# Optimization experiments

Measured on AMD Instinct MI355X. Metric: run time of the kernel, lower is better.

Reference implementation:

```python
import jax, jax.numpy as jnp
import numpy as np


def conv2d(x, w, b, pad):
    out = jax.lax.conv_general_dilated(x, w, (1, 1), ((pad, pad), (pad, pad)),
                                       dimension_numbers=('NCHW', 'OIHW', 'NCHW'))
    return out + b[None, :, None, None]


def silu(x):
    return x * jax.nn.sigmoid(x)


def group_norm(x, g, b, groups, eps=1e-5):
    B, C, H, W = x.shape
    xg = x.reshape(B, groups, C // groups, H, W)
    m = xg.mean(axis=(2, 3, 4), keepdims=True)
    v = xg.var(axis=(2, 3, 4), keepdims=True)
    xg = (xg - m) * jax.lax.rsqrt(v + eps)
    return xg.reshape(B, C, H, W) * g[None, :, None, None] + b[None, :, None, None]


def snake_cumsum(off):
    # off: [B,K,H,W]. Center kernel point has zero offset; points accumulate
    # outward from center (the 'snake' bend), as in DSCNet.
    K = off.shape[1]
    c = K // 2
    upper = jnp.cumsum(off[:, c + 1:], axis=1)
    lower = jnp.flip(jnp.cumsum(jnp.flip(off[:, :c], axis=1), axis=1), axis=1)
    return jnp.concatenate([lower, jnp.zeros_like(off[:, :1]), upper], axis=1)


def bilinear_gather(img, ys, xs):
    # img [B,C,H,W]; ys,xs [B,K,H,W] float coords -> sampled [B,C,K,H,W]
    B, C, H, W = img.shape
    K = ys.shape[1]
    ys = jnp.clip(ys, 0.0, H - 1.0)
    xs = jnp.clip(xs, 0.0, W - 1.0)
    y0f = jnp.floor(ys)
    x0f = jnp.floor(xs)
    wy = (ys - y0f)[:, None]  # [B,1,K,H,W]
    wx = (xs - x0f)[:, None]
    y0 = y0f.astype(jnp.int32)
    x0 = x0f.astype(jnp.int32)
    y1 = jnp.minimum(y0 + 1, H - 1)
    x1 = jnp.minimum(x0 + 1, W - 1)
    flat = img.reshape(B, C, H * W)

    def gat(yi, xi):
        idx = (yi * W + xi).reshape(B, -1)  # [B, K*H*W]
        g = jnp.take_along_axis(flat, idx[:, None, :], axis=2)
        return g.reshape(B, C, K, H, W)

    return (gat(y0, x0) * (1 - wy) * (1 - wx) + gat(y0, x1) * (1 - wy) * wx
            + gat(y1, x0) * wy * (1 - wx) + gat(y1, x1) * wy * wx)


def dsconv(x, off_w, off_b, dsc_w, dsc_b, gn_g, gn_b, morph, extend_scope=1.0):
    # Dynamic snake conv for one morphology.
    # morph 0: kernel spreads along x, bends in y; morph 1: opposite.
    B, C, H, W = x.shape
    K = dsc_w.shape[-1]
    c = K // 2
    off = jnp.tanh(conv2d(x, off_w, off_b, pad=1))  # [B,2K,H,W]; BN folded into conv bias
    bend = snake_cumsum(off[:, :K] if morph == 0 else off[:, K:])  # [B,K,H,W]
    spread = (jnp.arange(K) - c).astype(x.dtype)[None, :, None, None]
    hh = jnp.arange(H, dtype=x.dtype)[None, None, :, None]
    ww = jnp.arange(W, dtype=x.dtype)[None, None, None, :]
    if morph == 0:
        ys = hh + extend_scope * bend
        xs = jnp.broadcast_to(ww + spread, ys.shape)
    else:
        xs = ww + extend_scope * bend
        ys = jnp.broadcast_to(hh + spread, xs.shape)
    sampled = bilinear_gather(x, ys, xs)  # [B,C,K,H,W]
    # k-point conv over the stacked snake axis == (K,1)/(1,K) conv with stride K
    out = jnp.einsum('bckhw,ock->bohw', sampled, dsc_w) + dsc_b[None, :, None, None]
    O = dsc_w.shape[0]
    return jax.nn.relu(group_norm(out, gn_g, gn_b, groups=O // 4))


def dysnake_conv(x, p):
    # DySnakeConv: standard conv + snake-x + snake-y, concat, 1x1 fuse
    kpad = p['conv0_w'].shape[-1] // 2
    a = silu(conv2d(x, p['conv0_w'], p['conv0_b'], pad=kpad))
    bx = dsconv(x, p['offx_w'], p['offx_b'], p['dscx_w'], p['dscx_b'], p['gnx_g'], p['gnx_b'], morph=0)
    by = dsconv(x, p['offy_w'], p['offy_b'], p['dscy_w'], p['dscy_b'], p['gny_g'], p['gny_b'], morph=1)
    cat = jnp.concatenate([a, bx, by], axis=1)  # [B,3*ouc,H,W]
    return silu(jnp.einsum('bchw,oc->bohw', cat, p['fuse_w']) + p['fuse_b'][None, :, None, None])


_PNAMES = ['conv0_w', 'conv0_b', 'offx_w', 'offx_b', 'dscx_w', 'dscx_b', 'gnx_g', 'gnx_b',
           'offy_w', 'offy_b', 'dscy_w', 'dscy_b', 'gny_g', 'gny_b', 'fuse_w', 'fuse_b']


def setup_inputs() -> dict:
    key = jax.random.key(0)
    ks = iter(jax.random.split(key, 64))

    def rn(shape, s=0.05):
        return jax.random.normal(next(ks), shape, dtype=jnp.float32) * s

    B, H, W = 8, 80, 80
    c1, c2, c_ = 256, 256, 128
    kk = 3

    def block(inc, ouc, pre):
        return {
            pre + 'conv0_w': rn((ouc, inc, kk, kk)), pre + 'conv0_b': rn((ouc,)),
            pre + 'offx_w': rn((2 * kk, inc, 3, 3)), pre + 'offx_b': rn((2 * kk,)),
            pre + 'dscx_w': rn((ouc, inc, kk)), pre + 'dscx_b': rn((ouc,)),
            pre + 'gnx_g': jnp.ones((ouc,), jnp.float32), pre + 'gnx_b': jnp.zeros((ouc,), jnp.float32),
            pre + 'offy_w': rn((2 * kk, inc, 3, 3)), pre + 'offy_b': rn((2 * kk,)),
            pre + 'dscy_w': rn((ouc, inc, kk)), pre + 'dscy_b': rn((ouc,)),
            pre + 'gny_g': jnp.ones((ouc,), jnp.float32), pre + 'gny_b': jnp.zeros((ouc,), jnp.float32),
            pre + 'fuse_w': rn((ouc, 3 * ouc)), pre + 'fuse_b': rn((ouc,)),
        }

    inp = {'x': jax.random.normal(next(ks), (B, c1, H, W), dtype=jnp.float32)}
    inp.update(block(c1, c_, 'cv1_'))
    inp.update(block(c_, c2, 'cv2_'))
    return inp


def reference(x, cv1_conv0_w, cv1_conv0_b, cv1_offx_w, cv1_offx_b, cv1_dscx_w, cv1_dscx_b,
              cv1_gnx_g, cv1_gnx_b, cv1_offy_w, cv1_offy_b, cv1_dscy_w, cv1_dscy_b,
              cv1_gny_g, cv1_gny_b, cv1_fuse_w, cv1_fuse_b,
              cv2_conv0_w, cv2_conv0_b, cv2_offx_w, cv2_offx_b, cv2_dscx_w, cv2_dscx_b,
              cv2_gnx_g, cv2_gnx_b, cv2_offy_w, cv2_offy_b, cv2_dscy_w, cv2_dscy_b,
              cv2_gny_g, cv2_gny_b, cv2_fuse_w, cv2_fuse_b):
    p1 = dict(zip(_PNAMES, (cv1_conv0_w, cv1_conv0_b, cv1_offx_w, cv1_offx_b, cv1_dscx_w, cv1_dscx_b,
                            cv1_gnx_g, cv1_gnx_b, cv1_offy_w, cv1_offy_b, cv1_dscy_w, cv1_dscy_b,
                            cv1_gny_g, cv1_gny_b, cv1_fuse_w, cv1_fuse_b)))
    p2 = dict(zip(_PNAMES, (cv2_conv0_w, cv2_conv0_b, cv2_offx_w, cv2_offx_b, cv2_dscx_w, cv2_dscx_b,
                            cv2_gnx_g, cv2_gnx_b, cv2_offy_w, cv2_offy_b, cv2_dscy_w, cv2_dscy_b,
                            cv2_gny_g, cv2_gny_b, cv2_fuse_w, cv2_fuse_b)))
    h = dysnake_conv(x, p1)
    h = dysnake_conv(h, p2)
    return x + h  # shortcut and c1 == c2
```

## Files before the change

kernel.cpp:

```cpp
#include <hip/hip_runtime.h>
#include <cstddef>

#define B_   8
#define H_   80
#define W_   80
#define HW   6400
#define W2   82
#define HW2  6724

typedef __attribute__((ext_vector_type(8)))  short short8;
typedef __attribute__((ext_vector_type(16))) float f32x16;

__device__ __forceinline__ float bf2f(ushort u) {
    return __uint_as_float(((unsigned)u) << 16);
}
__device__ __forceinline__ ushort f2bf(float f) {
    unsigned u = __float_as_uint(f);
    u += 0x7FFF + ((u >> 16) & 1);
    return (ushort)(u >> 16);
}
__device__ __forceinline__ f32x16 mfma16(short8 a, short8 b, f32x16 c) {
    return __builtin_amdgcn_mfma_f32_32x32x16_bf16(a, b, c, 0, 0, 0);
}
__device__ __forceinline__ void async16(const void* g, void* l) {
    __builtin_amdgcn_global_load_lds(
        (const __attribute__((address_space(1))) unsigned int*)g,
        (__attribute__((address_space(3))) unsigned int*)l, 16, 0, 0);
}
__device__ __forceinline__ const ushort* frag_ptr(const ushort* sbuf, int row, int c8l) {
    return sbuf + row * 64 + ((c8l ^ (row & 7)) << 3);
}

__global__ __launch_bounds__(256) void transpose_x_kernel(
    const float* __restrict__ x, ushort* __restrict__ xp, int C) {
    __shared__ float s[64][65];
    int hw0 = blockIdx.x * 64, c0 = blockIdx.y * 64, b = blockIdx.z;
    int t = threadIdx.x;
    int hl = t & 63, cq = t >> 6;
    #pragma unroll
    for (int i = 0; i < 16; i++) {
        int cl = cq * 16 + i;
        s[cl][hl] = x[((size_t)(b * C + c0 + cl)) * HW + hw0 + hl];
    }
    __syncthreads();
    int cl = t & 63, hq = t >> 6;
    #pragma unroll
    for (int i = 0; i < 16; i++) {
        int hl2 = hq * 16 + i;
        int hw = hw0 + hl2;
        int h = hw / W_, w = hw - h * W_;
        xp[((size_t)(b * HW2 + (h + 1) * W2 + w + 1)) * C + c0 + cl] = f2bf(s[cl][hl2]);
    }
}

__global__ __launch_bounds__(256) void final_add_kernel(
    const float* __restrict__ x, const ushort* __restrict__ h2,
    float* __restrict__ out, int C) {
    __shared__ float s[64][65];
    int hw0 = blockIdx.x * 64, c0 = blockIdx.y * 64, b = blockIdx.z;
    int t = threadIdx.x;
    int cl = t & 63, hq = t >> 6;
    #pragma unroll
    for (int i = 0; i < 16; i++) {
        int hl = hq * 16 + i;
        s[cl][hl] = bf2f(h2[((size_t)(b * HW + hw0 + hl)) * C + c0 + cl]);
    }
    __syncthreads();
    int hl = t & 63, cq = t >> 6;
    #pragma unroll
    for (int i = 0; i < 16; i++) {
        int cl2 = cq * 16 + i;
        size_t o = ((size_t)(b * C + c0 + cl2)) * HW + hw0 + hl;
        out[o] = x[o] + s[cl2][hl];
    }
}

__global__ void wprep_kernel(const float* __restrict__ src,
                             ushort* __restrict__ dst, int OC, int CIN, int T) {
    int idx = blockIdx.x * 256 + threadIdx.x;
    if (idx >= OC * CIN * T) return;
    int oc = idx / (CIN * T);
    int r = idx - oc * CIN * T;
    int ci = r / T, t_ = r - ci * T;
    dst[((size_t)oc * T + t_) * CIN + ci] = f2bf(src[idx]);
}

__global__ void wprep_off_kernel(const float* __restrict__ wx_,
                                 const float* __restrict__ bx_,
                                 const float* __restrict__ wy_,
                                 const float* __restrict__ by_,
                                 ushort* __restrict__ dst,
                                 float* __restrict__ bdst, int CIN) {
    int idx = blockIdx.x * 256 + threadIdx.x;
    if (idx < 4) {
        const int chs[4] = {0, 2, 3, 5};
        bdst[idx] = (idx < 2) ? bx_[chs[idx]] : by_[chs[idx]];
    }
    if (idx >= 32 * 9 * CIN) return;
    int oc = idx / (9 * CIN);
    int r = idx - oc * 9 * CIN;
    int tap = r / CIN, ci = r - tap * CIN;
    float v = 0.f;
    if (oc < 4) {
        const int chs[4] = {0, 2, 3, 5};
        const float* src = (oc < 2) ? wx_ : wy_;
        v = src[((size_t)chs[oc] * CIN + ci) * 9 + tap];
    }
    dst[idx] = f2bf(v);
}

__global__ __launch_bounds__(256, 2) void off_conv_mfma_kernel(
    const ushort* __restrict__ xp, const ushort* __restrict__ wB,
    const float* __restrict__ bias, float* __restrict__ off4, int CIN) {
    __shared__ ushort s_x[162 * 64];
    __shared__ ushort s_w[144 * 64];
    int tid = threadIdx.x;
    int ty0 = (blockIdx.x / 5) * 16, tx0 = (blockIdx.x % 5) * 16;
    int b = blockIdx.y;
    int lane = tid & 63, wid = tid >> 6;
    int l31 = lane & 31, kg = lane >> 5;
    int pym[2], pxm[2];
    #pragma unroll
    for (int mf = 0; mf < 2; mf++) {
        int p = wid * 64 + mf * 32 + l31;
        pym[mf] = p >> 4; pxm[mf] = p & 15;
    }
    f32x16 acc[2] = {};
    for (int c0 = 0; c0 < CIN; c0 += 32) {
        __syncthreads();
        for (int u = tid; u < 1296; u += 256) {
            int pid = u >> 2, ci8 = u & 3;
            int r = pid / 18, c = pid - r * 18;
            int py = ty0 + r, px = tx0 + c;
            uint4 v = *(const uint4*)(xp + ((size_t)(b * HW2 + py * W2 + px)) * CIN
                                      + c0 + ci8 * 8);
            int row = pid >> 1;
            int phys = (((pid & 1) << 2) + ci8) ^ (row & 7);
            *(uint4*)(s_x + row * 64 + phys * 8) = v;
        }
        for (int cc = wid; cc < 18; cc += 4) {
            int L = cc * 64 + lane;
            int row = L >> 3, phys = L & 7;
            int logical = phys ^ (row & 7);
            int tap = row >> 4, ocp = row & 15;
            int oc = ocp * 2 + (logical >> 2), ci8 = logical & 3;
            async16(wB + ((size_t)oc * 9 + tap) * CIN + c0 + ci8 * 8,
                    s_w + (size_t)L * 8);
        }
        __syncthreads();
        #pragma unroll
        for (int tap = 0; tap < 9; tap++) {
            int dy = tap / 3, dx = tap - dy * 3;
            int wrow = tap * 16 + (l31 >> 1);
            #pragma unroll
            for (int ks = 0; ks < 2; ks++) {
                int blk = ks * 2 + kg;
                int wphys = (((l31 & 1) << 2) + blk) ^ (wrow & 7);
                short8 bfr = *(const short8*)(s_w + wrow * 64 + wphys * 8);
                #pragma unroll
                for (int mf = 0; mf < 2; mf++) {
                    int pix = (pym[mf] + dy) * 18 + (pxm[mf] + dx);
                    int xrow = pix >> 1;
                    int xphys = (((pix & 1) << 2) + blk) ^ (xrow & 7);
                    short8 afr = *(const short8*)(s_x + xrow * 64 + xphys * 8);
                    acc[mf] = mfma16(afr, bfr, acc[mf]);
                }
            }
        }
    }
    int oc = l31;
    if (oc < 4) {
        float bb = bias[oc];
        #pragma unroll
        for (int mf = 0; mf < 2; mf++) {
            #pragma unroll
            for (int reg = 0; reg < 16; reg++) {
                int row = (reg & 3) + 8 * (reg >> 2) + 4 * kg;
                int p = wid * 64 + mf * 32 + row;
                int y = ty0 + (p >> 4), x = tx0 + (p & 15);
                off4[((size_t)b * 4 + oc) * HW + y * W_ + x] = tanhf(acc[mf][reg] + bb);
            }
        }
    }
}

__global__ __launch_bounds__(256, 4) void conv3x3_gemm_kernel(
    const ushort* __restrict__ xp, const ushort* __restrict__ wB,
    const float* __restrict__ bias, ushort* __restrict__ out,
    int CIN, int OC) {
    __shared__ ushort s_a[128 * 64];
    __shared__ ushort s_b[128 * 64];
    int tid = threadIdx.x;
    int m0 = blockIdx.x * 128, n0 = blockIdx.y * 128;
    int b = m0 / HW, hw0 = m0 - b * HW;
    int lane = tid & 63, wid = tid >> 6;
    int l31 = lane & 31, kg = lane >> 5;
    int wm = wid >> 1, wn = wid & 1;
    const ushort* xpb = xp + (size_t)b * HW2 * CIN;
    const ushort* asrc[4];
    #pragma unroll
    for (int j = 0; j < 4; j++) {
        int s = (wid * 4 + j) * 64 + lane;
        int r = s >> 3, c8p = s & 7;
        int c8l = c8p ^ (r & 7);
        int hw = hw0 + r;
        int h = hw / W_, w = hw - h * W_;
        asrc[j] = xpb + ((size_t)((h + 1) * W2 + (w + 1))) * CIN + c8l * 8;
    }
    f32x16 acc[2][2] = {};
    int K = 9 * CIN, nk = K >> 6;
    int tap = 0, cioff = 0;
    for (int kc = 0; kc < nk; kc++) {
        int kg64 = kc << 6;
        int dy = tap / 3, dx = tap - dy * 3;
        int soff = ((dy - 1) * W2 + (dx - 1)) * CIN + cioff;
        __syncthreads();
        #pragma unroll
        for (int j = 0; j < 4; j++) {
            int s = (wid * 4 + j) * 64 + lane;
            int r = s >> 3, c8p = s & 7;
            int c8l = c8p ^ (r & 7);
            async16(wB + (size_t)(n0 + r) * K + kg64 + c8l * 8, s_b + s * 8);
            async16(asrc[j] + soff, s_a + s * 8);
        }
        __syncthreads();
        #pragma unroll
        for (int ks = 0; ks < 4; ks++) {
            int c8l = ks * 2 + kg;
            short8 af0 = *(const short8*)frag_ptr(s_a, wm * 64 + l31, c8l);
            short8 af1 = *(const short8*)frag_ptr(s_a, wm * 64 + 32 + l31, c8l);
            short8 bf0 = *(const short8*)frag_ptr(s_b, wn * 64 + l31, c8l);
            short8 bf1 = *(const short8*)frag_ptr(s_b, wn * 64 + 32 + l31, c8l);
            acc[0][0] = mfma16(af0, bf0, acc[0][0]);
            acc[0][1] = mfma16(af0, bf1, acc[0][1]);
            acc[1][0] = mfma16(af1, bf0, acc[1][0]);
            acc[1][1] = mfma16(af1, bf1, acc[1][1]);
        }
        cioff += 64;
        if (cioff == CIN) { cioff = 0; tap++; }
    }
    #pragma unroll
    for (int nf = 0; nf < 2; nf++) {
        int n = n0 + wn * 64 + nf * 32 + l31;
        float bb = bias[n];
        #pragma unroll
        for (int mf = 0; mf < 2; mf++) {
            #pragma unroll
            for (int reg = 0; reg < 16; reg++) {
                int row = (reg & 3) + 8 * (reg >> 2) + 4 * kg;
                int m = m0 + wm * 64 + mf * 32 + row;
                float v = acc[mf][nf][reg] + bb;
                v = v / (1.f + expf(-v));
                out[(size_t)m * OC + n] = f2bf(v);
            }
        }
    }
}

__global__ __launch_bounds__(256, 4) void dsc_gemm_kernel(
    const ushort* __restrict__ xp, const float* __restrict__ off4,
    const ushort* __restrict__ Bwx, const float* __restrict__ biasx,
    ushort* __restrict__ outx,
    const ushort* __restrict__ Bwy, const float* __restrict__ biasy,
    ushort* __restrict__ outy, float* __restrict__ stat, int CIN, int OC) {
    __shared__ ushort s_a[128 * 64];
    __shared__ ushort s_b[128 * 64];
    __shared__ int   s_i0[3][128];
    __shared__ int   s_i1[3][128];
    __shared__ float s_wl[3][128];
    int tid = threadIdx.x;
    int morph = blockIdx.z;
    const ushort* Bw = morph ? Bwy : Bwx;
    const float* bias = morph ? biasy : biasx;
    ushort* out = morph ? outy : outx;
    float* statm = stat + (size_t)morph * B_ * 256 * 2;
    int m0 = blockIdx.x * 128, n0 = blockIdx.y * 128;
    int b = m0 / HW, hw0 = m0 - b * HW;
    for (int u = tid; u < 384; u += 256) {
        int k3 = u >> 7, r = u & 127;
        int hw = hw0 + r;
        int h = hw / W_, w = hw - h * W_;
        float bend = 0.f;
        if (k3 != 1) {
            int mp = (morph ? 2 : 0) + (k3 >> 1);
            bend = off4[((size_t)b * 4 + mp) * HW + hw];
        }
        int i0, i1; float wl;
        if (morph == 0) {
            float ys = fminf(fmaxf((float)h + bend, 0.f), 79.f);
            float y0f = floorf(ys); wl = ys - y0f;
            int y0 = (int)y0f, y1 = min(y0 + 1, 79);
            int xk = min(max(w + k3 - 1, 0), 79);
            i0 = (y0 + 1) * W2 + xk + 1; i1 = (y1 + 1) * W2 + xk + 1;
        } else {
            float xs = fminf(fmaxf((float)w + bend, 0.f), 79.f);
            float x0f = floorf(xs); wl = xs - x0f;
            int x0 = (int)x0f, x1 = min(x0 + 1, 79);
            int yk = min(max(h + k3 - 1, 0), 79);
            i0 = (yk + 1) * W2 + x0 + 1; i1 = (yk + 1) * W2 + x1 + 1;
        }
        s_i0[k3][r] = i0; s_i1[k3][r] = i1; s_wl[k3][r] = wl;
    }
    int lane = tid & 63, wid = tid >> 6;
    int l31 = lane & 31, kg = lane >> 5;
    int wm = wid >> 1, wn = wid & 1;
    f32x16 acc[2][2] = {};
    int K = 3 * CIN, nk = K >> 6;
    const ushort* xb = xp + (size_t)b * HW2 * CIN;
    for (int kc = 0; kc < nk; kc++) {
        int kg64 = kc << 6;
        int k3 = kg64 / CIN;
        int cioff = kg64 - k3 * CIN;
        __syncthreads();
        #pragma unroll
        for (int j = 0; j < 4; j++) {
            int s = (wid * 4 + j) * 64 + lane;
            int r = s >> 3, c8p = s & 7;
            int c8l = c8p ^ (r & 7);
            async16(Bw + (size_t)(n0 + r) * K + kg64 + c8l * 8, s_b + s * 8);
        }
        #pragma unroll
        for (int i = 0; i < 4; i++) {
            int s = i * 256 + tid;
            int r = s >> 3, c8p = s & 7;
            int c8l = c8p ^ (r & 7);
            int ci = cioff + c8l * 8;
            float wl = s_wl[k3][r];
            uint4 u0 = *(const uint4*)(xb + (size_t)s_i0[k3][r] * CIN + ci);
            uint4 u1 = *(const uint4*)(xb + (size_t)s_i1[k3][r] * CIN + ci);
            const ushort* p0 = (const ushort*)&u0;
            const ushort* p1 = (const ushort*)&u1;
            ushort tv[8];
            #pragma unroll
            for (int j = 0; j < 8; j++) {
                float f0 = bf2f(p0[j]);
                tv[j] = f2bf(f0 + (bf2f(p1[j]) - f0) * wl);
            }
            *(uint4*)(s_a + s * 8) = *(uint4*)tv;
        }
        __syncthreads();
        #pragma unroll
        for (int ks = 0; ks < 4; ks++) {
            int c8l = ks * 2 + kg;
            short8 af0 = *(const short8*)frag_ptr(s_a, wm * 64 + l31, c8l);
            short8 af1 = *(const short8*)frag_ptr(s_a, wm * 64 + 32 + l31, c8l);
            short8 bf0 = *(const short8*)frag_ptr(s_b, wn * 64 + l31, c8l);
            short8 bf1 = *(const short8*)frag_ptr(s_b, wn * 64 + 32 + l31, c8l);
            acc[0][0] = mfma16(af0, bf0, acc[0][0]);
            acc[0][1] = mfma16(af0, bf1, acc[0][1]);
            acc[1][0] = mfma16(af1, bf0, acc[1][0]);
            acc[1][1] = mfma16(af1, bf1, acc[1][1]);
        }
    }
    #pragma unroll
    for (int nf = 0; nf < 2; nf++) {
        int n = n0 + wn * 64 + nf * 32 + l31;
        float bb = bias[n];
        float ssum = 0.f, ssq = 0.f;
        #pragma unroll
        for (int mf = 0; mf < 2; mf++) {
            #pragma unroll
            for (int reg = 0; reg < 16; reg++) {
                int row = (reg & 3) + 8 * (reg >> 2) + 4 * kg;
                int m = m0 + wm * 64 + mf * 32 + row;
                float v = acc[mf][nf][reg] + bb;
                ssum += v; ssq += v * v;
                out[(size_t)m * OC + n] = f2bf(v);
            }
        }
        ssum += __shfl_xor(ssum, 32);
        ssq  += __shfl_xor(ssq, 32);
        if (kg == 0) {
            float* st = statm + ((size_t)b * OC + n) * 2;
            atomicAdd(st, ssum);
            atomicAdd(st + 1, ssq);
        }
    }
}

__global__ __launch_bounds__(256, 4) void gemm128_kernel(
    const ushort* __restrict__ a0, const ushort* __restrict__ a1,
    const ushort* __restrict__ a2, int part_k,
    const ushort* __restrict__ Bw, int K, int N,
    const float* __restrict__ bias, ushort* __restrict__ out, int epi_silu,
    int out_pad) {
    __shared__ ushort s_a[128 * 64];
    __shared__ ushort s_b[128 * 64];
    int tid = threadIdx.x;
    int m0 = blockIdx.x * 128, n0 = blockIdx.y * 128;
    int lane = tid & 63, wid = tid >> 6;
    int l31 = lane & 31, kg = lane >> 5;
    int wm = wid >> 1, wn = wid & 1;
    f32x16 acc[2][2] = {};
    int nk = K >> 6;
    for (int kc = 0; kc < nk; kc++) {
        int kg64 = kc << 6;
        int part = kg64 / part_k;
        int koff = kg64 - part * part_k;
        const ushort* ap = (part == 0) ? a0 : (part == 1 ? a1 : a2);
        __syncthreads();
        #pragma unroll
        for (int j = 0; j < 4; j++) {
            int s = (wid * 4 + j) * 64 + lane;
            int r = s >> 3, c8p = s & 7;
            int c8l = c8p ^ (r & 7);
            async16(ap + (size_t)(m0 + r) * part_k + koff + c8l * 8, s_a + s * 8);
            async16(Bw + (size_t)(n0 + r) * K + kg64 + c8l * 8, s_b + s * 8);
        }
        __syncthreads();
        #pragma unroll
        for (int ks = 0; ks < 4; ks++) {
            int c8l = ks * 2 + kg;
            short8 af0 = *(const short8*)frag_ptr(s_a, wm * 64 + l31, c8l);
            short8 af1 = *(const short8*)frag_ptr(s_a, wm * 64 + 32 + l31, c8l);
            short8 bf0 = *(const short8*)frag_ptr(s_b, wn * 64 + l31, c8l);
            short8 bf1 = *(const short8*)frag_ptr(s_b, wn * 64 + 32 + l31, c8l);
            acc[0][0] = mfma16(af0, bf0, acc[0][0]);
            acc[0][1] = mfma16(af0, bf1, acc[0][1]);
            acc[1][0] = mfma16(af1, bf0, acc[1][0]);
            acc[1][1] = mfma16(af1, bf1, acc[1][1]);
        }
    }
    #pragma unroll
    for (int nf = 0; nf < 2; nf++) {
        int n = n0 + wn * 64 + nf * 32 + l31;
        float bb = bias[n];
        #pragma unroll
        for (int mf = 0; mf < 2; mf++) {
            #pragma unroll
            for (int reg = 0; reg < 16; reg++) {
                int row = (reg & 3) + 8 * (reg >> 2) + 4 * kg;
                int m = m0 + wm * 64 + mf * 32 + row;
                float v = acc[mf][nf][reg] + bb;
                if (epi_silu) v = v / (1.f + expf(-v));
                size_t mm = (size_t)m;
                if (out_pad) {
                    int bb_ = m / HW, hw = m - bb_ * HW;
                    int h = hw / W_, w = hw - h * W_;
                    mm = (size_t)bb_ * HW2 + (h + 1) * W2 + w + 1;
                }
                out[mm * N + n] = f2bf(v);
            }
        }
    }
}

__global__ void gn_finalize_kernel(const float* __restrict__ stat,
                                   const float* __restrict__ gx,
                                   const float* __restrict__ bx,
                                   const float* __restrict__ gy,
                                   const float* __restrict__ by,
                                   float* __restrict__ scx, float* __restrict__ shx,
                                   float* __restrict__ scy, float* __restrict__ shy,
                                   int C) {
    int idx = blockIdx.x * 256 + threadIdx.x;
    if (idx >= B_ * C) return;
    int which = blockIdx.y;
    const float* gamma = which ? gy : gx;
    const float* beta  = which ? by : bx;
    float* sc = which ? scy : scx;
    float* sh = which ? shy : shx;
    int b = idx / C, c = idx - b * C;
    const float* st = stat + (size_t)which * B_ * 256 * 2
                    + ((size_t)b * C + (c & ~3)) * 2;
    float s  = st[0] + st[2] + st[4] + st[6];
    float sq = st[1] + st[3] + st[5] + st[7];
    float mean = s / (4.f * HW);
    float var = sq / (4.f * HW) - mean * mean;
    float rs = rsqrtf(var + 1e-5f);
    float scale = rs * gamma[c];
    sc[idx] = scale;
    sh[idx] = beta[c] - mean * scale;
}

__global__ __launch_bounds__(256) void gn_apply_kernel(
    ushort* __restrict__ bqx, ushort* __restrict__ bqy,
    const float* __restrict__ scx, const float* __restrict__ shx,
    const float* __restrict__ scy, const float* __restrict__ shy, int C) {
    ushort* bq = blockIdx.y ? bqy : bqx;
    const float* sc = blockIdx.y ? scy : scx;
    const float* sh = blockIdx.y ? shy : shx;
    size_t e = ((size_t)blockIdx.x * 256 + threadIdx.x) * 8;
    int c = (int)(e % C);
    int b = (int)(e / ((size_t)HW * C));
    const float* scb = sc + (size_t)b * C + c;
    const float* shb = sh + (size_t)b * C + c;
    uint4 v = *(const uint4*)(bq + e);
    const ushort* sv = (const ushort*)&v;
    ushort tv[8];
    #pragma unroll
    for (int j = 0; j < 8; j++)
        tv[j] = f2bf(fmaxf(bf2f(sv[j]) * scb[j] + shb[j], 0.f));
    *(uint4*)(bq + e) = *(uint4*)tv;
}

struct BlkBuf {
    ushort *xp, *abuf, *bqx, *bqy, *hout;
    float *off4, *stat, *scx, *shx, *scy, *shy, *boff;
    ushort *wc, *wdx, *wdy, *wf, *woff;
};

static void run_block(const BlkBuf& B, int CIN, int OC,
                      const float* const* P, int out_pad, hipStream_t stream) {
    dim3 blk(256);
    hipMemsetAsync(B.stat, 0, (size_t)2 * B_ * 256 * 2 * 4, stream);
    off_conv_mfma_kernel<<<dim3(25, B_), blk, 0, stream>>>(
        B.xp, B.woff, B.boff, B.off4, CIN);
    conv3x3_gemm_kernel<<<dim3(B_ * HW / 128, OC / 128), blk, 0, stream>>>(
        B.xp, B.wc, P[1], B.abuf, CIN, OC);
    dsc_gemm_kernel<<<dim3(400, OC / 128, 2), blk, 0, stream>>>(
        B.xp, B.off4, B.wdx, P[5], B.bqx, B.wdy, P[11], B.bqy, B.stat, CIN, OC);
    int fgrid = (B_ * OC + 255) / 256;
    gn_finalize_kernel<<<dim3(fgrid, 2), blk, 0, stream>>>(
        B.stat, P[6], P[7], P[12], P[13], B.scx, B.shx, B.scy, B.shy, OC);
    gn_apply_kernel<<<dim3((B_ * HW * OC) / 2048, 2), blk, 0, stream>>>(
        B.bqx, B.bqy, B.scx, B.shx, B.scy, B.shy, OC);
    gemm128_kernel<<<dim3(400, OC / 128), blk, 0, stream>>>(
        B.abuf, B.bqx, B.bqy, OC, B.wf, 3 * OC, OC, P[15], B.hout, 1, out_pad);
}

extern "C" void kernel_launch(void* const* d_in, const int* in_sizes, int n_in,
                              void* d_out, int out_size, void* d_ws, size_t ws_size,
                              hipStream_t stream) {
    const float* x = (const float*)d_in[0];
    const float* P1[16];
    const float* P2[16];
    for (int i = 0; i < 16; i++) {
        P1[i] = (const float*)d_in[1 + i];
        P2[i] = (const float*)d_in[17 + i];
    }
    char* base = (char*)d_ws;
    size_t off = 0;
    auto alloc = [&](size_t bytes) -> char* {
        off = (off + 255) & ~(size_t)255;
        char* p = base + off;
        off += bytes;
        return p;
    };
    ushort* xp1  = (ushort*)alloc((size_t)B_ * HW2 * 256 * 2);
    ushort* xp2  = (ushort*)alloc((size_t)B_ * HW2 * 128 * 2);
    ushort* abuf = (ushort*)alloc((size_t)B_ * HW * 256 * 2);
    ushort* bqx  = (ushort*)alloc((size_t)B_ * HW * 256 * 2);
    ushort* bqy  = (ushort*)alloc((size_t)B_ * HW * 256 * 2);
    float*  off4 = (float*)alloc((size_t)B_ * 4 * HW * 4);
    float*  stat = (float*)alloc((size_t)2 * B_ * 256 * 2 * 4);
    float*  scx  = (float*)alloc(B_ * 256 * 4);
    float*  shx  = (float*)alloc(B_ * 256 * 4);
    float*  scy  = (float*)alloc(B_ * 256 * 4);
    float*  shy  = (float*)alloc(B_ * 256 * 4);
    ushort* wc1  = (ushort*)alloc((size_t)128 * 9 * 256 * 2);
    ushort* wc2  = (ushort*)alloc((size_t)256 * 9 * 128 * 2);
    ushort* wdx1 = (ushort*)alloc((size_t)128 * 3 * 256 * 2);
    ushort* wdy1 = (ushort*)alloc((size_t)128 * 3 * 256 * 2);
    ushort* wdx2 = (ushort*)alloc((size_t)256 * 3 * 128 * 2);
    ushort* wdy2 = (ushort*)alloc((size_t)256 * 3 * 128 * 2);
    ushort* wf1  = (ushort*)alloc((size_t)128 * 384 * 2);
    ushort* wf2  = (ushort*)alloc((size_t)256 * 768 * 2);
    ushort* wo1  = (ushort*)alloc((size_t)32 * 9 * 256 * 2);
    ushort* wo2  = (ushort*)alloc((size_t)32 * 9 * 128 * 2);
    float*  bo1  = (float*)alloc(32 * 4);
    float*  bo2  = (float*)alloc(32 * 4);
    ushort* h2 = xp1;

    hipMemsetAsync(xp1, 0, (size_t)B_ * HW2 * 256 * 2, stream);
    hipMemsetAsync(xp2, 0, (size_t)B_ * HW2 * 128 * 2, stream);

    dim3 blk(256);
    auto wp = [&](const float* s, ushort* d, int OC, int CIN, int T) {
        int n = OC * CIN * T;
        wprep_kernel<<<(n + 255) / 256, blk, 0, stream>>>(s, d, OC, CIN, T);
    };
    wp(P1[0], wc1, 128, 256, 9);
    wp(P1[4], wdx1, 128, 256, 3);
    wp(P1[10], wdy1, 128, 256, 3);
    wp(P1[14], wf1, 128, 384, 1);
    wp(P2[0], wc2, 256, 128, 9);
    wp(P2[4], wdx2, 256, 128, 3);
    wp(P2[10], wdy2, 256, 128, 3);
    wp(P2[14], wf2, 256, 768, 1);
    wprep_off_kernel<<<(32 * 9 * 256 + 255) / 256, blk, 0, stream>>>(
        P1[2], P1[3], P1[8], P1[9], wo1, bo1, 256);
    wprep_off_kernel<<<(32 * 9 * 128 + 255) / 256, blk, 0, stream>>>(
        P2[2], P2[3], P2[8], P2[9], wo2, bo2, 128);

    transpose_x_kernel<<<dim3(100, 4, B_), blk, 0, stream>>>(x, xp1, 256);

    BlkBuf B1 = {xp1, abuf, bqx, bqy, xp2, off4, stat, scx, shx, scy, shy,
                 bo1, wc1, wdx1, wdy1, wf1, wo1};
    run_block(B1, 256, 128, P1, 1, stream);

    BlkBuf B2 = {xp2, abuf, bqx, bqy, h2, off4, stat, scx, shx, scy, shy,
                 bo2, wc2, wdx2, wdy2, wf2, wo2};
    run_block(B2, 128, 256, P2, 0, stream);

    final_add_kernel<<<dim3(100, 4, B_), blk, 0, stream>>>(x, h2, (float*)d_out, 256);
}
```

Baseline: 584.1 us.

## Skip interpolation for center snake tap, zero only halos, pack bf16 conversion

The center kernel tap of the snake conv has zero offset, so its A-tile is now loaded directly from the padded input with async global-to-LDS copies instead of two gathers plus a lerp. The full-buffer memsets of the padded activations are replaced by a kernel that zeros only the halo border. The remaining lerp path converts pairs of floats with a packed bf16 conversion instruction instead of manual rounding. Correctness relies on the center offset being exactly zero and on interior padded pixels always being overwritten before use.

```diff
diff --git a/kernel.cpp b/kernel.cpp
--- a/kernel.cpp
+++ b/kernel.cpp
@@ -29,6 +29,23 @@
 }
 __device__ __forceinline__ const ushort* frag_ptr(const ushort* sbuf, int row, int c8l) {
     return sbuf + row * 64 + ((c8l ^ (row & 7)) << 3);
+}
+
+__global__ __launch_bounds__(256) void halo_zero_kernel(
+    ushort* __restrict__ xp, int C) {
+    int idx = blockIdx.x * 256 + threadIdx.x;
+    int slots = C >> 3;
+    int total = B_ * 324 * slots;
+    if (idx >= total) return;
+    int sl = idx % slots;
+    int t = idx / slots;
+    int p = t % 324;
+    int b = t / 324;
+    int h, w;
+    if (p < 164) { h = (p < 82) ? 0 : 81; w = p % 82; }
+    else { int q = p - 164; w = (q < 80) ? 0 : 81; h = 1 + (q % 80); }
+    *(uint4*)(xp + ((size_t)(b * HW2 + h * W2 + w)) * C + sl * 8) =
+        make_uint4(0, 0, 0, 0);
 }
 
 __global__ __launch_bounds__(256) void transpose_x_kernel(
@@ -304,9 +321,19 @@
     int lane = tid & 63, wid = tid >> 6;
     int l31 = lane & 31, kg = lane >> 5;
     int wm = wid >> 1, wn = wid & 1;
+    const ushort* xb = xp + (size_t)b * HW2 * CIN;
+    const ushort* asrcC[4];
+    #pragma unroll
+    for (int j = 0; j < 4; j++) {
+        int s = (wid * 4 + j) * 64 + lane;
+        int r = s >> 3, c8p = s & 7;
+        int c8l = c8p ^ (r & 7);
+        int hw = hw0 + r;
+        int h = hw / W_, w = hw - h * W_;
+        asrcC[j] = xb + ((size_t)((h + 1) * W2 + (w + 1))) * CIN + c8l * 8;
+    }
     f32x16 acc[2][2] = {};
     int K = 3 * CIN, nk = K >> 6;
-    const ushort* xb = xp + (size_t)b * HW2 * CIN;
     for (int kc = 0; kc < nk; kc++) {
         int kg64 = kc << 6;
         int k3 = kg64 / CIN;
@@ -319,24 +346,36 @@
             int c8l = c8p ^ (r & 7);
             async16(Bw + (size_t)(n0 + r) * K + kg64 + c8l * 8, s_b + s * 8);
         }
-        #pragma unroll
-        for (int i = 0; i < 4; i++) {
-            int s = i * 256 + tid;
-            int r = s >> 3, c8p = s & 7;
-            int c8l = c8p ^ (r & 7);
-            int ci = cioff + c8l * 8;
-            float wl = s_wl[k3][r];
-            uint4 u0 = *(const uint4*)(xb + (size_t)s_i0[k3][r] * CIN + ci);
-            uint4 u1 = *(const uint4*)(xb + (size_t)s_i1[k3][r] * CIN + ci);
-            const ushort* p0 = (const ushort*)&u0;
-            const ushort* p1 = (const ushort*)&u1;
-            ushort tv[8];
+        if (k3 == 1) {
             #pragma unroll
-            for (int j = 0; j < 8; j++) {
-                float f0 = bf2f(p0[j]);
-                tv[j] = f2bf(f0 + (bf2f(p1[j]) - f0) * wl);
+            for (int j = 0; j < 4; j++) {
+                int s = (wid * 4 + j) * 64 + lane;
+                async16(asrcC[j] + cioff, s_a + s * 8);
             }
-            *(uint4*)(s_a + s * 8) = *(uint4*)tv;
+        } else {
+            #pragma unroll
+            for (int i = 0; i < 4; i++) {
+                int s = i * 256 + tid;
+                int r = s >> 3, c8p = s & 7;
+                int c8l = c8p ^ (r & 7);
+                int ci = cioff + c8l * 8;
+                float wl = s_wl[k3][r];
+                uint4 u0 = *(const uint4*)(xb + (size_t)s_i0[k3][r] * CIN + ci);
+                uint4 u1 = *(const uint4*)(xb + (size_t)s_i1[k3][r] * CIN + ci);
+                const ushort* p0 = (const ushort*)&u0;
+                const ushort* p1 = (const ushort*)&u1;
+                uint ov[4];
+                #pragma unroll
+                for (int j = 0; j < 4; j++) {
+                    float a0 = bf2f(p0[2 * j]),     b0 = bf2f(p1[2 * j]);
+                    float a1 = bf2f(p0[2 * j + 1]), b1 = bf2f(p1[2 * j + 1]);
+                    float r0 = a0 + (b0 - a0) * wl;
+                    float r1 = a1 + (b1 - a1) * wl;
+                    asm("v_cvt_pk_bf16_f32 %0, %1, %2"
+                        : "=v"(ov[j]) : "v"(r0), "v"(r1));
+                }
+                *(uint4*)(s_a + s * 8) = *(uint4*)ov;
+            }
         }
         __syncthreads();
         #pragma unroll
@@ -562,10 +601,10 @@
     float*  bo2  = (float*)alloc(32 * 4);
     ushort* h2 = xp1;
 
-    hipMemsetAsync(xp1, 0, (size_t)B_ * HW2 * 256 * 2, stream);
-    hipMemsetAsync(xp2, 0, (size_t)B_ * HW2 * 128 * 2, stream);
-
     dim3 blk(256);
+    halo_zero_kernel<<<(B_ * 324 * 32 + 255) / 256, blk, 0, stream>>>(xp1, 256);
+    halo_zero_kernel<<<(B_ * 324 * 16 + 255) / 256, blk, 0, stream>>>(xp2, 128);
+
     auto wp = [&](const float* s, ushort* d, int OC, int CIN, int T) {
         int n = OC * CIN * T;
         wprep_kernel<<<(n + 255) / 256, blk, 0, stream>>>(s, d, OC, CIN, T);
```

New measurement: 576.4 us. Within noise of the previous version (-1.3%).
